# Optimization experiments

Measured on AMD Instinct MI355X. Metric: run time of the kernel, lower is better.

The kernel has to match this reference:

```python
import jax, jax.numpy as jnp
import numpy as np

GAMMA = 1.0
N, M, D = 8192, 8192, 256


def setup_inputs() -> dict:
    key = jax.random.key(0)
    kx, ky = jax.random.split(key)
    x = jax.random.normal(kx, (N, D), dtype=jnp.float32)
    y = jax.random.normal(ky, (M, D), dtype=jnp.float32)
    return {"x": x, "y": y}


def reference(x, y):
    # Pairwise squared distances without materializing the (n, m, d) diff
    x2 = jnp.sum(x * x, axis=-1)              # (n,)
    y2 = jnp.sum(y * y, axis=-1)              # (m,)
    xy = jnp.einsum('nd,md->nm', x, y)        # (n, m)
    dist_sq = x2[:, None] + y2[None, :] - 2.0 * xy
    # clamp tiny negative values from cancellation to preserve exp(-g*d2)<=1
    dist_sq = jnp.maximum(dist_sq, 0.0)
    return jnp.exp(-GAMMA * dist_sq)
```

## Files before the change

kernel.cpp:

```cpp
#include <hip/hip_runtime.h>
#include <hip/hip_bf16.h>

typedef __attribute__((ext_vector_type(4))) float f32x4;
typedef __attribute__((ext_vector_type(8))) short bf16x8;
typedef __attribute__((ext_vector_type(16))) float f32x16;
typedef long i64t;

#define MSZ 8192
#define D_DIM 256
#define PM 64
#define PN 64
#define NT2 16

#define GLOAD_LDS(g, s) __builtin_amdgcn_global_load_lds( \
    (const __attribute__((address_space(1))) unsigned int*)(g), \
    (__attribute__((address_space(3))) unsigned int*)(s), 16, 0, 0)

__device__ __forceinline__ unsigned short f2bf(float f) {
  __hip_bfloat16 h = __float2bfloat16(f);
  unsigned short u; __builtin_memcpy(&u, &h, 2); return u;
}

__global__ __launch_bounds__(256)
void prep_fp8(const float* __restrict__ X, const float* __restrict__ Y,
              unsigned char* __restrict__ Xq, unsigned char* __restrict__ Yq,
              float* __restrict__ x2, float* __restrict__ y2) {
  int gw = (blockIdx.x * 256 + threadIdx.x) >> 6;
  int l = threadIdx.x & 63;
  int row = gw & (MSZ - 1);
  const float* src = (gw < MSZ ? X : Y) + (size_t)row * D_DIM + l * 4;
  f32x4 v = *(const f32x4*)src;
  float ss = v[0]*v[0] + v[1]*v[1] + v[2]*v[2] + v[3]*v[3];
  int p = __builtin_amdgcn_cvt_pk_fp8_f32(v[0], v[1], 0, false);
  p = __builtin_amdgcn_cvt_pk_fp8_f32(v[2], v[3], p, true);
  unsigned char* dst = (gw < MSZ ? Xq : Yq) + (size_t)row * D_DIM + l * 4;
  *(unsigned int*)dst = (unsigned int)p;
  #pragma unroll
  for (int m = 1; m < 64; m <<= 1) ss += __shfl_xor(ss, m);
  if (l == 0) (gw < MSZ ? x2 : y2)[row] = ss;
}

__global__ __launch_bounds__(256, 4)
void rbf_main(const unsigned char* __restrict__ Xq, const unsigned char* __restrict__ Yq,
              const float* __restrict__ X2, const float* __restrict__ Y2,
              float* __restrict__ Out) {
  __shared__ __align__(16) unsigned char Al[PM * D_DIM];
  __shared__ __align__(16) unsigned char Bl[PN * D_DIM];
  __shared__ float sx2[PM];
  __shared__ float sy2l[NT2 * PN];

  int bid = blockIdx.x;
  int swz = (bid & 7) * 128 + (bid >> 3);
  int bm = swz >> 3;
  int cg = swz & 7;
  int rowBase = bm * PM;
  int colBase = cg * (PN * NT2);

  int tid = threadIdx.x;
  int l = tid & 63;
  int w = tid >> 6;
  int wr = w >> 1, wc = w & 1;
  int sk = l & 15;

  if (tid < PM) sx2[tid] = X2[rowBase + tid];
  *(f32x4*)&sy2l[tid * 4] = *(const f32x4*)&Y2[colBase + tid * 4];

  #pragma unroll
  for (int q = 0; q < 4; ++q) {
    int c = tid + 256 * q;
    int row = c >> 4, g = c & 15;
    GLOAD_LDS(Xq + (size_t)(rowBase + row) * D_DIM + ((g ^ (row & 15)) << 4), Al + c * 16);
  }
  #pragma unroll
  for (int q = 0; q < 4; ++q) {
    int c = tid + 256 * q;
    int row = c >> 4, g = c & 15;
    GLOAD_LDS(Yq + (size_t)(colBase + row) * D_DIM + ((g ^ (row & 15)) << 4), Bl + c * 16);
  }
  asm volatile("s_waitcnt vmcnt(0)" ::: "memory");
  __syncthreads();

  const unsigned char* Abase = Al + (wr * 32 + (l & 31)) * D_DIM + ((l >> 5) << 3);
  const unsigned char* Bbase = Bl + (wc * 32 + (l & 31)) * D_DIM + ((l >> 5) << 3);
  int rb0 = wr * 32 + 4 * (l >> 5);
  float sxv[16];
  #pragma unroll
  for (int q = 0; q < 16; ++q)
    sxv[q] = sx2[rb0 + (q & 3) + 8 * (q >> 2)];

  #pragma unroll 1
  for (int tt = 0; tt < NT2; ++tt) {
    if (tt) {
      asm volatile("s_waitcnt vmcnt(16)" ::: "memory");
      __builtin_amdgcn_s_barrier();
    }
    __builtin_amdgcn_sched_barrier(0);

    f32x16 acc = {};
    #pragma unroll
    for (int kk = 0; kk < 16; ++kk) {
      int ca = (kk ^ sk) << 4;
      i64t a = *(const i64t*)(Abase + ca);
      i64t b = *(const i64t*)(Bbase + ca);
      acc = __builtin_amdgcn_mfma_f32_32x32x16_fp8_fp8(a, b, acc, 0, 0, 0);
    }
    __builtin_amdgcn_s_barrier();
    asm volatile("" ::: "memory");

    if (tt + 1 < NT2) {
      int colN = colBase + (tt + 1) * PN;
      #pragma unroll
      for (int q = 0; q < 4; ++q) {
        int c = tid + 256 * q;
        int row = c >> 4, g = c & 15;
        GLOAD_LDS(Yq + (size_t)(colN + row) * D_DIM + ((g ^ (row & 15)) << 4), Bl + c * 16);
      }
    }
    asm volatile("" ::: "memory");

    float sy = sy2l[tt * PN + wc * 32 + (l & 31)];
    float* base = Out + (size_t)(rowBase + rb0) * MSZ + colBase + tt * PN + wc * 32 + (l & 31);
    #pragma unroll
    for (int q = 0; q < 16; ++q) {
      int rpat = (q & 3) + 8 * (q >> 2);
      float d = fmaf(-2.0f, acc[q], sxv[q] + sy);
      base[(size_t)rpat * MSZ] = __expf(-fmaxf(d, 0.0f));
    }
    asm volatile("" ::: "memory");
  }
}

__global__ __launch_bounds__(256, 2)
void rbf_mfma_kernel(const float* __restrict__ X, const float* __restrict__ Y,
                     float* __restrict__ Out) {
  __shared__ unsigned short As[128 * 64];
  __shared__ unsigned short Bs[128 * 64];
  __shared__ float sx2[128];
  __shared__ float sy2[128];
  int bid = blockIdx.x;
  int cpx = gridDim.x >> 3;
  int swz = (bid & 7) * cpx + (bid >> 3);
  int bm = swz >> 6, bn = swz & 63;
  int rowBase = bm * 128, colBase = bn * 128;
  int tid = threadIdx.x;
  int l = tid & 63;
  int w = tid >> 6;
  int wr = w >> 1, wc = w & 1;
  f32x4 acc[4][4] = {};
  float assq[4] = {0.f,0.f,0.f,0.f};
  float bssq[4] = {0.f,0.f,0.f,0.f};
  for (int ks = 0; ks < D_DIM / 64; ++ks) {
    if (ks) __syncthreads();
    #pragma unroll
    for (int p = 0; p < 4; ++p) {
      int c = tid + 256 * p;
      int r = c >> 3;
      int kc = c & 7;
      const float* gx = X + (size_t)(rowBase + r) * D_DIM + ks * 64 + kc * 8;
      const float* gy = Y + (size_t)(colBase + r) * D_DIM + ks * 64 + kc * 8;
      f32x4 xa = *(const f32x4*)gx;
      f32x4 xb = *(const f32x4*)(gx + 4);
      f32x4 ya = *(const f32x4*)gy;
      f32x4 yb = *(const f32x4*)(gy + 4);
      #pragma unroll
      for (int j = 0; j < 4; ++j) {
        assq[p] += xa[j]*xa[j] + xb[j]*xb[j];
        bssq[p] += ya[j]*ya[j] + yb[j]*yb[j];
      }
      union { bf16x8 v; unsigned short u[8]; } pa, pb;
      #pragma unroll
      for (int j = 0; j < 4; ++j) {
        pa.u[j] = f2bf(xa[j]);  pa.u[j+4] = f2bf(xb[j]);
        pb.u[j] = f2bf(ya[j]);  pb.u[j+4] = f2bf(yb[j]);
      }
      int boff = (r * 128 + kc * 16) ^ ((r & 7) << 4);
      *(bf16x8*)((char*)As + boff) = pa.v;
      *(bf16x8*)((char*)Bs + boff) = pb.v;
    }
    __syncthreads();
    #pragma unroll
    for (int kk = 0; kk < 2; ++kk) {
      bf16x8 af[4], bfv[4];
      #pragma unroll
      for (int i = 0; i < 4; ++i) {
        int ra = wr*64 + i*16 + (l & 15);
        int offa = (ra * 128 + kk*64 + (l >> 4) * 16) ^ ((ra & 7) << 4);
        af[i] = *(bf16x8*)((char*)As + offa);
        int rb = wc*64 + i*16 + (l & 15);
        int offb = (rb * 128 + kk*64 + (l >> 4) * 16) ^ ((rb & 7) << 4);
        bfv[i] = *(bf16x8*)((char*)Bs + offb);
      }
      #pragma unroll
      for (int i = 0; i < 4; ++i)
        #pragma unroll
        for (int j = 0; j < 4; ++j)
          acc[i][j] = __builtin_amdgcn_mfma_f32_16x16x32_bf16(af[i], bfv[j], acc[i][j], 0, 0, 0);
    }
  }
  #pragma unroll
  for (int p = 0; p < 4; ++p) {
    float a = assq[p], b = bssq[p];
    a += __shfl_xor(a, 1); b += __shfl_xor(b, 1);
    a += __shfl_xor(a, 2); b += __shfl_xor(b, 2);
    a += __shfl_xor(a, 4); b += __shfl_xor(b, 4);
    if ((tid & 7) == 0) {
      int r = (tid >> 3) + 32 * p;
      sx2[r] = a;
      sy2[r] = b;
    }
  }
  __syncthreads();
  #pragma unroll
  for (int i = 0; i < 4; ++i)
    #pragma unroll
    for (int j = 0; j < 4; ++j)
      #pragma unroll
      for (int q = 0; q < 4; ++q) {
        int rn = wr*64 + i*16 + (l >> 4) * 4 + q;
        int cm = wc*64 + j*16 + (l & 15);
        float d2 = sx2[rn] + sy2[cm] - 2.0f * acc[i][j][q];
        Out[(size_t)(rowBase + rn) * MSZ + (colBase + cm)] = __expf(-fmaxf(d2, 0.0f));
      }
}

extern "C" void kernel_launch(void* const* d_in, const int* in_sizes, int n_in,
                              void* d_out, int out_size, void* d_ws, size_t ws_size,
                              hipStream_t stream) {
  const float* X = (const float*)d_in[0];
  const float* Y = (const float*)d_in[1];
  float* Out = (float*)d_out;
  const size_t QB = (size_t)MSZ * D_DIM;
  const size_t NEED = QB * 2 + (size_t)MSZ * 4 * 2;
  if (ws_size >= NEED) {
    unsigned char* Xq = (unsigned char*)d_ws;
    unsigned char* Yq = Xq + QB;
    float* x2 = (float*)(Yq + QB);
    float* y2 = x2 + MSZ;
    prep_fp8<<<dim3(4096), dim3(256), 0, stream>>>(X, Y, Xq, Yq, x2, y2);
    rbf_main<<<dim3(1024), dim3(256), 0, stream>>>(Xq, Yq, x2, y2, Out);
  } else {
    rbf_mfma_kernel<<<dim3(64 * 64), dim3(256), 0, stream>>>(X, Y, Out);
  }
}
```

Before: 59.24 us.

## Fuse X fp8 quantization into main kernel and use nontemporal output stores

The X-side fp8 quantization and squared-norm computation move out of the prep kernel and into the main kernel's A-tile load. Each block now reads its 64 fp32 rows of X directly, converts them to fp8 into swizzled LDS, and reduces the norms with shuffles. The prep kernel now only handles Y, which halves its work and removes the Xq/x2 workspace round-trip. Output stores become nontemporal to avoid polluting cache with the 256MB result, at the cost of each X row being read and converted by 8 blocks and a synchronous load on the prologue path.

New measurement: 83.45 us. 1.41x slower.

```diff
diff --git a/kernel.cpp b/kernel.cpp
--- a/kernel.cpp
+++ b/kernel.cpp
@@ -2,6 +2,7 @@
 #include <hip/hip_bf16.h>
 
 typedef __attribute__((ext_vector_type(4))) float f32x4;
+typedef __attribute__((ext_vector_type(4))) int i32x4;
 typedef __attribute__((ext_vector_type(8))) short bf16x8;
 typedef __attribute__((ext_vector_type(16))) float f32x16;
 typedef long i64t;
@@ -22,28 +23,24 @@
 }
 
 __global__ __launch_bounds__(256)
-void prep_fp8(const float* __restrict__ X, const float* __restrict__ Y,
-              unsigned char* __restrict__ Xq, unsigned char* __restrict__ Yq,
-              float* __restrict__ x2, float* __restrict__ y2) {
+void prep_y(const float* __restrict__ Y, unsigned char* __restrict__ Yq,
+            float* __restrict__ y2) {
   int gw = (blockIdx.x * 256 + threadIdx.x) >> 6;
   int l = threadIdx.x & 63;
-  int row = gw & (MSZ - 1);
-  const float* src = (gw < MSZ ? X : Y) + (size_t)row * D_DIM + l * 4;
+  const float* src = Y + (size_t)gw * D_DIM + l * 4;
   f32x4 v = *(const f32x4*)src;
   float ss = v[0]*v[0] + v[1]*v[1] + v[2]*v[2] + v[3]*v[3];
   int p = __builtin_amdgcn_cvt_pk_fp8_f32(v[0], v[1], 0, false);
   p = __builtin_amdgcn_cvt_pk_fp8_f32(v[2], v[3], p, true);
-  unsigned char* dst = (gw < MSZ ? Xq : Yq) + (size_t)row * D_DIM + l * 4;
-  *(unsigned int*)dst = (unsigned int)p;
+  *(unsigned int*)(Yq + (size_t)gw * D_DIM + l * 4) = (unsigned int)p;
   #pragma unroll
   for (int m = 1; m < 64; m <<= 1) ss += __shfl_xor(ss, m);
-  if (l == 0) (gw < MSZ ? x2 : y2)[row] = ss;
+  if (l == 0) y2[gw] = ss;
 }
 
 __global__ __launch_bounds__(256, 4)
-void rbf_main(const unsigned char* __restrict__ Xq, const unsigned char* __restrict__ Yq,
-              const float* __restrict__ X2, const float* __restrict__ Y2,
-              float* __restrict__ Out) {
+void rbf_main(const float* __restrict__ X, const unsigned char* __restrict__ Yq,
+              const float* __restrict__ Y2, float* __restrict__ Out) {
   __shared__ __align__(16) unsigned char Al[PM * D_DIM];
   __shared__ __align__(16) unsigned char Bl[PN * D_DIM];
   __shared__ float sx2[PM];
@@ -62,21 +59,39 @@
   int wr = w >> 1, wc = w & 1;
   int sk = l & 15;
 
-  if (tid < PM) sx2[tid] = X2[rowBase + tid];
   *(f32x4*)&sy2l[tid * 4] = *(const f32x4*)&Y2[colBase + tid * 4];
 
-  #pragma unroll
-  for (int q = 0; q < 4; ++q) {
-    int c = tid + 256 * q;
-    int row = c >> 4, g = c & 15;
-    GLOAD_LDS(Xq + (size_t)(rowBase + row) * D_DIM + ((g ^ (row & 15)) << 4), Al + c * 16);
-  }
   #pragma unroll
   for (int q = 0; q < 4; ++q) {
     int c = tid + 256 * q;
     int row = c >> 4, g = c & 15;
     GLOAD_LDS(Yq + (size_t)(colBase + row) * D_DIM + ((g ^ (row & 15)) << 4), Bl + c * 16);
   }
+
+  {
+    int arow = tid >> 2;
+    int part = tid & 3;
+    const float* xsrc = X + (size_t)(rowBase + arow) * D_DIM + part * 64;
+    float ss = 0.0f;
+    #pragma unroll
+    for (int g4 = 0; g4 < 4; ++g4) {
+      i32x4 pk;
+      #pragma unroll
+      for (int d = 0; d < 4; ++d) {
+        f32x4 v = *(const f32x4*)(xsrc + g4 * 16 + d * 4);
+        ss += v[0]*v[0] + v[1]*v[1] + v[2]*v[2] + v[3]*v[3];
+        int p = __builtin_amdgcn_cvt_pk_fp8_f32(v[0], v[1], 0, false);
+        p = __builtin_amdgcn_cvt_pk_fp8_f32(v[2], v[3], p, true);
+        pk[d] = p;
+      }
+      int gg = part * 4 + g4;
+      *(i32x4*)(Al + arow * D_DIM + ((gg ^ (arow & 15)) << 4)) = pk;
+    }
+    ss += __shfl_xor(ss, 1);
+    ss += __shfl_xor(ss, 2);
+    if (part == 0) sx2[arow] = ss;
+  }
+
   asm volatile("s_waitcnt vmcnt(0)" ::: "memory");
   __syncthreads();
 
@@ -124,7 +139,7 @@
     for (int q = 0; q < 16; ++q) {
       int rpat = (q & 3) + 8 * (q >> 2);
       float d = fmaf(-2.0f, acc[q], sxv[q] + sy);
-      base[(size_t)rpat * MSZ] = __expf(-fmaxf(d, 0.0f));
+      __builtin_nontemporal_store(__expf(-fmaxf(d, 0.0f)), base + (size_t)rpat * MSZ);
     }
     asm volatile("" ::: "memory");
   }
@@ -230,14 +245,12 @@
   const float* Y = (const float*)d_in[1];
   float* Out = (float*)d_out;
   const size_t QB = (size_t)MSZ * D_DIM;
-  const size_t NEED = QB * 2 + (size_t)MSZ * 4 * 2;
+  const size_t NEED = QB + (size_t)MSZ * 4;
   if (ws_size >= NEED) {
-    unsigned char* Xq = (unsigned char*)d_ws;
-    unsigned char* Yq = Xq + QB;
-    float* x2 = (float*)(Yq + QB);
-    float* y2 = x2 + MSZ;
-    prep_fp8<<<dim3(4096), dim3(256), 0, stream>>>(X, Y, Xq, Yq, x2, y2);
-    rbf_main<<<dim3(1024), dim3(256), 0, stream>>>(Xq, Yq, x2, y2, Out);
+    unsigned char* Yq = (unsigned char*)d_ws;
+    float* y2 = (float*)(Yq + QB);
+    prep_y<<<dim3(2048), dim3(256), 0, stream>>>(Y, Yq, y2);
+    rbf_main<<<dim3(1024), dim3(256), 0, stream>>>(X, Yq, y2, Out);
   } else {
     rbf_mfma_kernel<<<dim3(64 * 64), dim3(256), 0, stream>>>(X, Y, Out);
   }
```

## Give each wave a private B buffer to remove block barriers in fp8 RBF loop

Applied to the files above, without the earlier changes.

Each wave now owns its own 32-column B tile in LDS and computes a 64x32 output tile (two MFMA accumulators sharing one B fragment) instead of a 32x32 tile. The per-tile block-wide s_barrier calls are removed, since waves only wait on their own global-to-LDS loads. Row norms are loaded straight from global into registers. This cuts the number of B tile loads and removes cross-wave synchronisation, at the cost of more LDS per block, more registers and lower occupancy (launch bounds go from 4 to 3 blocks).

Measured after the change: 64.32 us. 1.09x slower.

```diff
diff --git a/kernel.cpp b/kernel.cpp
--- a/kernel.cpp
+++ b/kernel.cpp
@@ -8,9 +8,6 @@
 
 #define MSZ 8192
 #define D_DIM 256
-#define PM 64
-#define PN 64
-#define NT2 16
 
 #define GLOAD_LDS(g, s) __builtin_amdgcn_global_load_lds( \
     (const __attribute__((address_space(1))) unsigned int*)(g), \
@@ -40,30 +37,35 @@
   if (l == 0) (gw < MSZ ? x2 : y2)[row] = ss;
 }
 
-__global__ __launch_bounds__(256, 4)
+__global__ __launch_bounds__(256, 3)
 void rbf_main(const unsigned char* __restrict__ Xq, const unsigned char* __restrict__ Yq,
               const float* __restrict__ X2, const float* __restrict__ Y2,
               float* __restrict__ Out) {
-  __shared__ __align__(16) unsigned char Al[PM * D_DIM];
-  __shared__ __align__(16) unsigned char Bl[PN * D_DIM];
-  __shared__ float sx2[PM];
-  __shared__ float sy2l[NT2 * PN];
+  __shared__ __align__(16) unsigned char Al[64 * D_DIM];
+  __shared__ __align__(16) unsigned char Bl[4][32 * D_DIM];
+  __shared__ float sy2l[1024];
 
   int bid = blockIdx.x;
   int swz = (bid & 7) * 128 + (bid >> 3);
   int bm = swz >> 3;
   int cg = swz & 7;
-  int rowBase = bm * PM;
-  int colBase = cg * (PN * NT2);
+  int rowBase = bm * 64;
+  int colBase = cg * 1024;
 
   int tid = threadIdx.x;
   int l = tid & 63;
   int w = tid >> 6;
-  int wr = w >> 1, wc = w & 1;
   int sk = l & 15;
-
-  if (tid < PM) sx2[tid] = X2[rowBase + tid];
+  int h = l >> 5;
+
   *(f32x4*)&sy2l[tid * 4] = *(const f32x4*)&Y2[colBase + tid * 4];
+
+  f32x4 sxv[2][4];
+  #pragma unroll
+  for (int i = 0; i < 2; ++i)
+    #pragma unroll
+    for (int g = 0; g < 4; ++g)
+      sxv[i][g] = *(const f32x4*)&X2[rowBase + i * 32 + g * 8 + 4 * h];
 
   #pragma unroll
   for (int q = 0; q < 4; ++q) {
@@ -72,59 +74,58 @@
     GLOAD_LDS(Xq + (size_t)(rowBase + row) * D_DIM + ((g ^ (row & 15)) << 4), Al + c * 16);
   }
   #pragma unroll
-  for (int q = 0; q < 4; ++q) {
-    int c = tid + 256 * q;
+  for (int q = 0; q < 8; ++q) {
+    int c = l + 64 * q;
     int row = c >> 4, g = c & 15;
-    GLOAD_LDS(Yq + (size_t)(colBase + row) * D_DIM + ((g ^ (row & 15)) << 4), Bl + c * 16);
+    GLOAD_LDS(Yq + (size_t)(colBase + w * 32 + row) * D_DIM + ((g ^ (row & 15)) << 4),
+              Bl[w] + c * 16);
   }
   asm volatile("s_waitcnt vmcnt(0)" ::: "memory");
   __syncthreads();
 
-  const unsigned char* Abase = Al + (wr * 32 + (l & 31)) * D_DIM + ((l >> 5) << 3);
-  const unsigned char* Bbase = Bl + (wc * 32 + (l & 31)) * D_DIM + ((l >> 5) << 3);
-  int rb0 = wr * 32 + 4 * (l >> 5);
-  float sxv[16];
-  #pragma unroll
-  for (int q = 0; q < 16; ++q)
-    sxv[q] = sx2[rb0 + (q & 3) + 8 * (q >> 2)];
+  const unsigned char* Abase = Al + (l & 31) * D_DIM + (h << 3);
+  const unsigned char* Bbase = Bl[w] + (l & 31) * D_DIM + (h << 3);
 
   #pragma unroll 1
-  for (int tt = 0; tt < NT2; ++tt) {
-    if (tt) {
-      asm volatile("s_waitcnt vmcnt(16)" ::: "memory");
-      __builtin_amdgcn_s_barrier();
-    }
-    __builtin_amdgcn_sched_barrier(0);
-
-    f32x16 acc = {};
+  for (int t = 0; t < 8; ++t) {
+    if (t) {
+      asm volatile("s_waitcnt vmcnt(32)" ::: "memory");
+      __builtin_amdgcn_sched_barrier(0);
+    }
+
+    f32x16 acc0 = {}, acc1 = {};
     #pragma unroll
     for (int kk = 0; kk < 16; ++kk) {
       int ca = (kk ^ sk) << 4;
-      i64t a = *(const i64t*)(Abase + ca);
-      i64t b = *(const i64t*)(Bbase + ca);
-      acc = __builtin_amdgcn_mfma_f32_32x32x16_fp8_fp8(a, b, acc, 0, 0, 0);
-    }
-    __builtin_amdgcn_s_barrier();
+      i64t b  = *(const i64t*)(Bbase + ca);
+      i64t a0 = *(const i64t*)(Abase + ca);
+      i64t a1 = *(const i64t*)(Abase + 32 * D_DIM + ca);
+      acc0 = __builtin_amdgcn_mfma_f32_32x32x16_fp8_fp8(a0, b, acc0, 0, 0, 0);
+      acc1 = __builtin_amdgcn_mfma_f32_32x32x16_fp8_fp8(a1, b, acc1, 0, 0, 0);
+    }
+    asm volatile("s_waitcnt lgkmcnt(0)" ::: "memory");
+    __builtin_amdgcn_sched_barrier(0);
+
+    if (t + 1 < 8) {
+      int colN = colBase + (t + 1) * 128 + w * 32;
+      #pragma unroll
+      for (int q = 0; q < 8; ++q) {
+        int c = l + 64 * q;
+        int row = c >> 4, g = c & 15;
+        GLOAD_LDS(Yq + (size_t)(colN + row) * D_DIM + ((g ^ (row & 15)) << 4), Bl[w] + c * 16);
+      }
+    }
     asm volatile("" ::: "memory");
 
-    if (tt + 1 < NT2) {
-      int colN = colBase + (tt + 1) * PN;
-      #pragma unroll
-      for (int q = 0; q < 4; ++q) {
-        int c = tid + 256 * q;
-        int row = c >> 4, g = c & 15;
-        GLOAD_LDS(Yq + (size_t)(colN + row) * D_DIM + ((g ^ (row & 15)) << 4), Bl + c * 16);
-      }
-    }
-    asm volatile("" ::: "memory");
-
-    float sy = sy2l[tt * PN + wc * 32 + (l & 31)];
-    float* base = Out + (size_t)(rowBase + rb0) * MSZ + colBase + tt * PN + wc * 32 + (l & 31);
+    float sy = sy2l[t * 128 + w * 32 + (l & 31)];
+    float* base = Out + (size_t)(rowBase + 4 * h) * MSZ + colBase + t * 128 + w * 32 + (l & 31);
     #pragma unroll
     for (int q = 0; q < 16; ++q) {
       int rpat = (q & 3) + 8 * (q >> 2);
-      float d = fmaf(-2.0f, acc[q], sxv[q] + sy);
-      base[(size_t)rpat * MSZ] = __expf(-fmaxf(d, 0.0f));
+      float d0 = fmaf(-2.0f, acc0[q], sxv[0][q >> 2][q & 3] + sy);
+      float d1 = fmaf(-2.0f, acc1[q], sxv[1][q >> 2][q & 3] + sy);
+      base[(size_t)rpat * MSZ]        = __expf(-fmaxf(d0, 0.0f));
+      base[(size_t)(rpat + 32) * MSZ] = __expf(-fmaxf(d1, 0.0f));
     }
     asm volatile("" ::: "memory");
   }
```
